# Performance work log

Measured on AMD Instinct MI355X. Metric: run time of the kernel, lower is better.

Reference implementation:

```python
import jax, jax.numpy as jnp
import numpy as np

B, S, D, H, T, R = 2, 2048, 768, 12, 64, 50
DH = D // H
EPS = 1e-12


def setup_inputs() -> dict:
    key = jax.random.key(0)
    ks = jax.random.split(key, 12)
    w = lambda k, shape: jax.random.normal(k, shape, jnp.float32) * 0.02
    inp = {
        "hidden_states": jax.random.normal(ks[0], (B, S, D), jnp.float32),
        "tag_emb": w(ks[1], (T, D)),
        "sa_wq": w(ks[2], (D, D)), "sa_bq": jnp.zeros((D,), jnp.float32),
        "sa_wk": w(ks[3], (D, D)), "sa_bk": jnp.zeros((D,), jnp.float32),
        "sa_wv": w(ks[4], (D, D)), "sa_bv": jnp.zeros((D,), jnp.float32),
        "sa_wo": w(ks[5], (D, D)), "sa_bo": jnp.zeros((D,), jnp.float32),
        "sa_ln_g": jnp.ones((D,), jnp.float32), "sa_ln_b": jnp.zeros((D,), jnp.float32),
        "ca_wq": w(ks[6], (D, D)), "ca_bq": jnp.zeros((D,), jnp.float32),
        "ca_wk": w(ks[7], (D, D)), "ca_bk": jnp.zeros((D,), jnp.float32),
        "ca_wv": w(ks[8], (D, D)), "ca_bv": jnp.zeros((D,), jnp.float32),
        "ca_wo": w(ks[9], (D, D)), "ca_bo": jnp.zeros((D,), jnp.float32),
        "ca_ln_g": jnp.ones((D,), jnp.float32), "ca_ln_b": jnp.zeros((D,), jnp.float32),
        "ff_w1": w(ks[10], (D, 3072)), "ff_b1": jnp.zeros((3072,), jnp.float32),
        "ff_w2": w(ks[11], (3072, D)), "ff_b2": jnp.zeros((D,), jnp.float32),
        "ff_ln_g": jnp.ones((D,), jnp.float32), "ff_ln_b": jnp.zeros((D,), jnp.float32),
    }
    return inp


def _layernorm(x, g, b):
    m = jnp.mean(x, axis=-1, keepdims=True)
    v = jnp.mean(jnp.square(x - m), axis=-1, keepdims=True)
    return (x - m) * jax.lax.rsqrt(v + EPS) * g + b


def _bert_attention(x, kv, mask, wq, bq, wk, bk, wv, bv, wo, bo, ln_g, ln_b):
    # BertSelfAttention: multi-head attn; mask (if any) is ADDED to scores (HF semantics).
    Bq, Sq = x.shape[0], x.shape[1]
    Sk = kv.shape[1]
    q = (x @ wq + bq).reshape(Bq, Sq, H, DH)
    k = (kv @ wk + bk).reshape(Bq, Sk, H, DH)
    v = (kv @ wv + bv).reshape(Bq, Sk, H, DH)
    scores = jnp.einsum("bqhd,bkhd->bhqk", q, k) / jnp.sqrt(jnp.float32(DH))
    if mask is not None:
        scores = scores + mask  # additive 0/1 band mask, as in the source
    probs = jax.nn.softmax(scores, axis=-1)
    ctx = jnp.einsum("bhqk,bkhd->bqhd", probs, v).reshape(Bq, Sq, D)
    # BertSelfOutput: dense + residual + LayerNorm
    return _layernorm(ctx @ wo + bo + x, ln_g, ln_b)


def reference(hidden_states, tag_emb,
              sa_wq, sa_bq, sa_wk, sa_bk, sa_wv, sa_bv, sa_wo, sa_bo, sa_ln_g, sa_ln_b,
              ca_wq, ca_bq, ca_wk, ca_bk, ca_wv, ca_bv, ca_wo, ca_bo, ca_ln_g, ca_ln_b,
              ff_w1, ff_b1, ff_w2, ff_b2, ff_ln_g, ff_ln_b):
    Sd = hidden_states.shape[1]
    # banded mask: tril(+R) * triu(-R) -> 1 inside window, 0 outside (added to scores)
    i = jnp.arange(Sd)
    band = (jnp.abs(i[:, None] - i[None, :]) <= R).astype(hidden_states.dtype)  # [S,S]
    attn_out = _bert_attention(hidden_states, hidden_states, band,
                               sa_wq, sa_bq, sa_wk, sa_bk, sa_wv, sa_bv,
                               sa_wo, sa_bo, sa_ln_g, sa_ln_b)
    tags = jnp.broadcast_to(tag_emb[None], (hidden_states.shape[0], T, D))
    attn_out = _bert_attention(attn_out, tags, None,
                               ca_wq, ca_bq, ca_wk, ca_bk, ca_wv, ca_bv,
                               ca_wo, ca_bo, ca_ln_g, ca_ln_b)
    # BertIntermediate + BertOutput (exact erf gelu as in HF)
    inter = jax.nn.gelu(attn_out @ ff_w1 + ff_b1, approximate=False)
    return _layernorm(inter @ ff_w2 + ff_b2 + attn_out, ff_ln_g, ff_ln_b)
```

## Files before the change

### kernel.cpp

```cpp
#include <hip/hip_runtime.h>
#include <cstdint>
#include <cstddef>


typedef __bf16 bf16;
typedef __bf16 bf16x8 __attribute__((ext_vector_type(8)));
typedef __bf16 bf16x4 __attribute__((ext_vector_type(4)));
typedef __bf16 bf16x2 __attribute__((ext_vector_type(2)));
typedef float  floatx4 __attribute__((ext_vector_type(4)));

__device__ __forceinline__ void glds16(const bf16* g, bf16* l) {
  __builtin_amdgcn_global_load_lds((const __attribute__((address_space(1))) void*)g,
                                   (__attribute__((address_space(3))) void*)l, 16, 0, 0);
}

__device__ __forceinline__ float fexp2(float x) {
  float r;
  asm("v_exp_f32 %0, %1" : "=v"(r) : "v"(x));
  return r;
}

__global__ __launch_bounds__(256) void k_prep(const float* __restrict__ sa_bq,
                                              const float* __restrict__ sa_bk,
                                              const float* __restrict__ sa_bv,
                                              const float* __restrict__ ca_bk,
                                              const float* __restrict__ ca_bv,
                                              const float* __restrict__ tag,
                                              float* __restrict__ bQKV,
                                              float* __restrict__ bKV2,
                                              bf16* __restrict__ tagp) {
  int b = blockIdx.x, t = threadIdx.x;
  if (b < 9) {
    int i = b * 256 + t;
    int s = i / 768, j = i - s * 768;
    const float* p = s == 0 ? sa_bq : (s == 1 ? sa_bk : sa_bv);
    bQKV[i] = p[j];
  } else if (b < 15) {
    int i = (b - 9) * 256 + t;
    int s = i / 768, j = i - s * 768;
    bKV2[i] = s == 0 ? ca_bk[j] : ca_bv[j];
  } else {
    int i = (b - 15) * 256 + t;
    if (i < 64 * 768) tagp[i] = (bf16)tag[i];
    else tagp[i] = (bf16)0.f;
  }
}

__global__ __launch_bounds__(256) void k_precast(const float* __restrict__ X,
                                                 bf16* __restrict__ Xb) {
  int i = (blockIdx.x * 256 + threadIdx.x) * 8;
  float4 a = *(const float4*)(X + i);
  float4 b4 = *(const float4*)(X + i + 4);
  bf16x8 o;
  o[0] = (bf16)a.x; o[1] = (bf16)a.y; o[2] = (bf16)a.z; o[3] = (bf16)a.w;
  o[4] = (bf16)b4.x; o[5] = (bf16)b4.y; o[6] = (bf16)b4.z; o[7] = (bf16)b4.w;
  *(bf16x8*)(Xb + i) = o;
}

__global__ __launch_bounds__(256) void k_transpose(const float* __restrict__ W,
                                                   bf16* __restrict__ Wt,
                                                   int K, int N) {
  __shared__ bf16 tile[64][72];
  int n0 = blockIdx.x * 64, k0 = blockIdx.y * 64;
  int t = threadIdx.x;
  int r = t >> 2, cg = (t & 3) * 16;
  const float* src = W + (size_t)(k0 + r) * N + n0 + cg;
  float tmp[16];
  *(float4*)&tmp[0]  = *(const float4*)(src);
  *(float4*)&tmp[4]  = *(const float4*)(src + 4);
  *(float4*)&tmp[8]  = *(const float4*)(src + 8);
  *(float4*)&tmp[12] = *(const float4*)(src + 12);
#pragma unroll
  for (int i = 0; i < 16; ++i) tile[r][cg + i] = (bf16)tmp[i];
  __syncthreads();
  bf16* dst = Wt + (size_t)(n0 + r) * K + k0 + cg;
#pragma unroll
  for (int g = 0; g < 2; ++g) {
    bf16x8 pack;
#pragma unroll
    for (int i = 0; i < 8; ++i) pack[i] = tile[cg + g * 8 + i][r];
    *(bf16x8*)(dst + g * 8) = pack;
  }
}

__global__ __launch_bounds__(256) void k_transpose4(const float* __restrict__ W0,
                                                    const float* __restrict__ W1,
                                                    const float* __restrict__ W2w,
                                                    const float* __restrict__ W3,
                                                    bf16* __restrict__ Wt) {
  __shared__ bf16 tile[64][72];
  int z = blockIdx.z;
  const float* W = z == 0 ? W0 : (z == 1 ? W1 : (z == 2 ? W2w : W3));
  bf16* dstb = Wt + (size_t)z * 768 * 768;
  int n0 = blockIdx.x * 64, k0 = blockIdx.y * 64;
  int t = threadIdx.x;
  int r = t >> 2, cg = (t & 3) * 16;
  const float* src = W + (size_t)(k0 + r) * 768 + n0 + cg;
  float tmp[16];
  *(float4*)&tmp[0]  = *(const float4*)(src);
  *(float4*)&tmp[4]  = *(const float4*)(src + 4);
  *(float4*)&tmp[8]  = *(const float4*)(src + 8);
  *(float4*)&tmp[12] = *(const float4*)(src + 12);
#pragma unroll
  for (int i = 0; i < 16; ++i) tile[r][cg + i] = (bf16)tmp[i];
  __syncthreads();
  bf16* dst = dstb + (size_t)(n0 + r) * 768 + k0 + cg;
#pragma unroll
  for (int g = 0; g < 2; ++g) {
    bf16x8 pack;
#pragma unroll
    for (int i = 0; i < 8; ++i) pack[i] = tile[cg + g * 8 + i][r];
    *(bf16x8*)(dst + g * 8) = pack;
  }
}

template <int BM, int BN, int KS, bool CF32>
__global__ __launch_bounds__(256) void k_gemm(const bf16* __restrict__ Ab,
                                              const bf16* __restrict__ Bt,
                                              const float* __restrict__ bias,
                                              void* __restrict__ Cv,
                                              void* __restrict__ Cv2,
                                              int M, int N, int K, int ld, int act) {
  constexpr int MT = BM / 32;
  constexpr int NT = BN / 32;
  __shared__ bf16 As[KS][BM * 32];
  __shared__ bf16 Bs[KS][BN * 32];
  int tid = threadIdx.x;
  int lane = tid & 63, wave = tid >> 6;
  int l16 = lane & 15, quad = lane >> 4;
  int wm = wave & 1, wn = wave >> 1;
  int m0 = blockIdx.x * BM, n0 = blockIdx.y * BN;
  int z = blockIdx.z;
  int arow = tid >> 2, acol = (tid & 3) * 8;
  int ldst = arow * 32 + acol;

  const bf16* Ap = Ab + (size_t)(m0 + arow) * ld + z * K + acol;
  const bf16* Bp = Bt + (size_t)(n0 + arow) * ld + z * K + acol;

  floatx4 acc[MT][NT];
#pragma unroll
  for (int i = 0; i < MT; ++i)
#pragma unroll
    for (int j = 0; j < NT; ++j) acc[i][j] = floatx4{0.f, 0.f, 0.f, 0.f};

  for (int k = 0; k < K; k += 32 * KS) {
    __syncthreads();
#pragma unroll
    for (int ks = 0; ks < KS; ++ks) {
      glds16(Bp + k + ks * 32, &Bs[ks][ldst]);
      if constexpr (BN == 128) glds16(Bp + (size_t)64 * ld + k + ks * 32, &Bs[ks][ldst + 2048]);
      glds16(Ap + k + ks * 32, &As[ks][ldst]);
      if constexpr (BM == 128) glds16(Ap + (size_t)64 * ld + k + ks * 32, &As[ks][ldst + 2048]);
    }
    __syncthreads();
#pragma unroll
    for (int ks = 0; ks < KS; ++ks) {
      bf16x8 a_frag[MT], b_frag[NT];
#pragma unroll
      for (int mt = 0; mt < MT; ++mt)
        a_frag[mt] = *(const bf16x8*)&As[ks][(wm * (BM / 2) + mt * 16 + l16) * 32 + quad * 8];
#pragma unroll
      for (int nt = 0; nt < NT; ++nt)
        b_frag[nt] = *(const bf16x8*)&Bs[ks][(wn * (BN / 2) + nt * 16 + l16) * 32 + quad * 8];
#pragma unroll
      for (int mt = 0; mt < MT; ++mt)
#pragma unroll
        for (int nt = 0; nt < NT; ++nt)
          acc[mt][nt] = __builtin_amdgcn_mfma_f32_16x16x32_bf16(a_frag[mt], b_frag[nt], acc[mt][nt], 0, 0, 0);
    }
  }

  void* Co = (z == 0) ? Cv : Cv2;
#pragma unroll
  for (int nt = 0; nt < NT; ++nt) {
    int col = n0 + wn * (BN / 2) + nt * 16 + l16;
    float bv = (z == 0) ? bias[col] : 0.f;
#pragma unroll
    for (int mt = 0; mt < MT; ++mt) {
#pragma unroll
      for (int r = 0; r < 4; ++r) {
        int row = m0 + wm * (BM / 2) + mt * 16 + quad * 4 + r;
        float v = acc[mt][nt][r] + bv;
        if (act) v = 0.5f * v * (1.f + erff(v * 0.70710678118654752f));
        if constexpr (CF32) ((float*)Co)[(size_t)row * N + col] = v;
        else ((bf16*)Co)[(size_t)row * N + col] = (bf16)v;
      }
    }
  }
}

__global__ __launch_bounds__(256) void k_attn_mfma(const bf16* __restrict__ Q, int ldq,
                                                   const bf16* __restrict__ Kp,
                                                   const bf16* __restrict__ Vp, int ldkv,
                                                   bf16* __restrict__ O,
                                                   int S, int Skv,
                                                   long long kv_bstride, int bandR) {
  const int NH = 12;
  int qt = blockIdx.x, bh = blockIdx.y;
  int bb = bh / NH, h = bh % NH;
  const bf16* Qb = Q + (size_t)bb * S * ldq + h * 64;
  const bf16* Kb = Kp + (size_t)bb * kv_bstride + h * 64;
  const bf16* Vb = Vp + (size_t)bb * kv_bstride + h * 64;
  bf16* Ob = O + (size_t)bb * S * 768 + h * 64;

  __shared__ __align__(16) char smem[47104];
  float* Obuf = (float*)smem;
  float* l0_arr = (float*)(smem + 16896);

  int tid = threadIdx.x, wave = tid >> 6, lane = tid & 63;
  int quad = lane >> 4, l16 = lane & 15;
  int qh = wave & 1, kh = wave >> 1;
  bf16 (*Psw)[40] = (bf16(*)[40])(smem + 36864 + wave * 2560);

  const float C1 = 0.18033688f;
  const float C2 = 1.44269504f;

  int r = tid >> 2, cg = (tid & 3) * 16;
  int vk0 = 2 * (tid & 31);
  int vd0 = 8 * (tid >> 5);
  int vcol = (vk0 + 16 * (vd0 >> 4)) & 63;

  bf16x8 aq[2][2];
#pragma unroll
  for (int mt = 0; mt < 2; ++mt) {
    const bf16* qsrc = Qb + (size_t)(qt * 64 + qh * 32 + mt * 16 + l16) * ldq;
#pragma unroll
    for (int ks = 0; ks < 2; ++ks) {
      bf16x8 t = *(const bf16x8*)(qsrc + ks * 32 + quad * 8);
#pragma unroll
      for (int e = 0; e < 8; ++e) t[e] = (bf16)((float)t[e] * C1);
      aq[mt][ks] = t;
    }
  }

  bf16x8 kr0, kr1, vr0, vr1;
  {
    const bf16* ksrc = Kb + (size_t)r * ldkv + cg;
    kr0 = *(const bf16x8*)ksrc;
    kr1 = *(const bf16x8*)(ksrc + 8);
    const bf16* vsrc = Vb + (size_t)vk0 * ldkv + vd0;
    vr0 = *(const bf16x8*)vsrc;
    vr1 = *(const bf16x8*)(vsrc + ldkv);
  }

  float l_part[2][4];
  floatx4 acc[2][4];
#pragma unroll
  for (int mt = 0; mt < 2; ++mt)
#pragma unroll
    for (int j = 0; j < 4; ++j) {
      l_part[mt][j] = 0.f;
      acc[mt][j] = floatx4{0.f, 0.f, 0.f, 0.f};
    }

  int qi0 = qt * 64 + qh * 32 + quad * 4;

  for (int kc = 0; kc < Skv; kc += 64) {
    int cur = (kc >> 6) & 1;
    bf16 (*Ks)[72] = (bf16(*)[72])(smem + cur * 9216);
    bf16 (*Vt)[72] = (bf16(*)[72])(smem + 18432 + cur * 9216);
    *(bf16x8*)&Ks[r][cg] = kr0;
    *(bf16x8*)&Ks[r][cg + 8] = kr1;
#pragma unroll
    for (int e = 0; e < 8; ++e) {
      bf16x2 p; p[0] = vr0[e]; p[1] = vr1[e];
      *(bf16x2*)&Vt[vd0 + e][vcol] = p;
    }
    if (kc + 64 < Skv) {
      const bf16* ksrc = Kb + (size_t)(kc + 64 + r) * ldkv + cg;
      kr0 = *(const bf16x8*)ksrc;
      kr1 = *(const bf16x8*)(ksrc + 8);
      const bf16* vsrc = Vb + (size_t)(kc + 64 + vk0) * ldkv + vd0;
      vr0 = *(const bf16x8*)vsrc;
      vr1 = *(const bf16x8*)(vsrc + ldkv);
    }
    __syncthreads();

    floatx4 s[2][2];
    __builtin_amdgcn_s_setprio(1);
#pragma unroll
    for (int kt = 0; kt < 2; ++kt) {
      bf16x8 bk0 = *(const bf16x8*)&Ks[kh * 32 + kt * 16 + l16][quad * 8];
      bf16x8 bk1 = *(const bf16x8*)&Ks[kh * 32 + kt * 16 + l16][32 + quad * 8];
#pragma unroll
      for (int mt = 0; mt < 2; ++mt) {
        floatx4 c = {0.f, 0.f, 0.f, 0.f};
        c = __builtin_amdgcn_mfma_f32_16x16x32_bf16(aq[mt][0], bk0, c, 0, 0, 0);
        c = __builtin_amdgcn_mfma_f32_16x16x32_bf16(aq[mt][1], bk1, c, 0, 0, 0);
        s[mt][kt] = c;
      }
    }
    __builtin_amdgcn_s_setprio(0);

    bool masked = (bandR >= 0) && (kc <= qt * 64 + 63 + bandR) &&
                  (kc + 63 >= qt * 64 - bandR);
    if (masked) {
#pragma unroll
      for (int kt = 0; kt < 2; ++kt) {
        int kj = kc + kh * 32 + kt * 16 + l16;
        int colp = (kt * 16 + l16 + 8 * quad) & 31;
#pragma unroll
        for (int mt = 0; mt < 2; ++mt)
#pragma unroll
          for (int rr = 0; rr < 4; ++rr) {
            int d = qi0 + mt * 16 + rr - kj; if (d < 0) d = -d;
            float e = fexp2(s[mt][kt][rr] + (d <= bandR ? C2 : 0.f));
            l_part[mt][rr] += e;
            Psw[mt * 16 + quad * 4 + rr][colp] = (bf16)e;
          }
      }
    } else {
#pragma unroll
      for (int kt = 0; kt < 2; ++kt) {
        int colp = (kt * 16 + l16 + 8 * quad) & 31;
#pragma unroll
        for (int mt = 0; mt < 2; ++mt)
#pragma unroll
          for (int rr = 0; rr < 4; ++rr) {
            float e = fexp2(s[mt][kt][rr]);
            l_part[mt][rr] += e;
            Psw[mt * 16 + quad * 4 + rr][colp] = (bf16)e;
          }
      }
    }

    bf16x8 ap[2];
#pragma unroll
    for (int mt = 0; mt < 2; ++mt)
      ap[mt] = *(const bf16x8*)&Psw[mt * 16 + l16][8 * ((quad + (l16 >> 2)) & 3)];
    __builtin_amdgcn_s_setprio(1);
#pragma unroll
    for (int nt = 0; nt < 4; ++nt) {
      bf16x8 bv = *(const bf16x8*)&Vt[nt * 16 + l16][(kh * 32 + quad * 8 + 16 * nt) & 63];
#pragma unroll
      for (int mt = 0; mt < 2; ++mt)
        acc[mt][nt] = __builtin_amdgcn_mfma_f32_16x16x32_bf16(ap[mt], bv, acc[mt][nt], 0, 0, 0);
    }
    __builtin_amdgcn_s_setprio(0);
  }

  float lr[2][4];
#pragma unroll
  for (int mt = 0; mt < 2; ++mt)
#pragma unroll
    for (int rr = 0; rr < 4; ++rr) {
      float t = l_part[mt][rr];
      t += __shfl_xor(t, 1);
      t += __shfl_xor(t, 2);
      t += __shfl_xor(t, 4);
      t += __shfl_xor(t, 8);
      lr[mt][rr] = t;
    }
  __syncthreads();
  if (kh == 0) {
#pragma unroll
    for (int mt = 0; mt < 2; ++mt)
#pragma unroll
      for (int nt = 0; nt < 4; ++nt)
#pragma unroll
        for (int rr = 0; rr < 4; ++rr)
          Obuf[(qh * 32 + mt * 16 + quad * 4 + rr) * 66 + nt * 16 + l16] = acc[mt][nt][rr];
    if (l16 == 0) {
#pragma unroll
      for (int mt = 0; mt < 2; ++mt)
#pragma unroll
        for (int rr = 0; rr < 4; ++rr)
          l0_arr[qh * 32 + mt * 16 + quad * 4 + rr] = lr[mt][rr];
    }
  }
  __syncthreads();
  if (kh == 1) {
#pragma unroll
    for (int mt = 0; mt < 2; ++mt)
#pragma unroll
      for (int rr = 0; rr < 4; ++rr) {
        int ql = qh * 32 + mt * 16 + quad * 4 + rr;
        float lt = lr[mt][rr] + l0_arr[ql];
        int qrow = qt * 64 + ql;
#pragma unroll
        for (int nt = 0; nt < 4; ++nt) {
          float o = (acc[mt][nt][rr] + Obuf[ql * 66 + nt * 16 + l16]) / lt;
          Ob[(size_t)qrow * 768 + nt * 16 + l16] = (bf16)o;
        }
      }
  }
}

template <typename TY, typename TR, typename TO>
__global__ __launch_bounds__(256) void k_add_ln(const TY* __restrict__ Y,
                                                const TR* __restrict__ X,
                                                const float* __restrict__ Y2,
                                                const float* __restrict__ g,
                                                const float* __restrict__ b,
                                                TO* __restrict__ out) {
  int wave = threadIdx.x >> 6, lane = threadIdx.x & 63;
  int row = blockIdx.x * 4 + wave;
  const TY* y = Y + (size_t)row * 768;
  const TR* x = X + (size_t)row * 768;
  float v[12];
  float s = 0.f, s2 = 0.f;
#pragma unroll
  for (int c = 0; c < 3; ++c) {
    int idx = c * 256 + lane * 4;
    float yv[4], xv[4];
    if constexpr (__is_same(TY, float)) {
      float4 t = *(const float4*)(y + idx);
      yv[0] = t.x; yv[1] = t.y; yv[2] = t.z; yv[3] = t.w;
    } else {
      bf16x4 t = *(const bf16x4*)(y + idx);
#pragma unroll
      for (int i = 0; i < 4; ++i) yv[i] = (float)t[i];
    }
    if constexpr (__is_same(TR, float)) {
      float4 t = *(const float4*)(x + idx);
      xv[0] = t.x; xv[1] = t.y; xv[2] = t.z; xv[3] = t.w;
    } else {
      bf16x4 t = *(const bf16x4*)(x + idx);
#pragma unroll
      for (int i = 0; i < 4; ++i) xv[i] = (float)t[i];
    }
    if (Y2 != nullptr) {
      float4 t2 = *(const float4*)(Y2 + (size_t)row * 768 + idx);
      xv[0] += t2.x; xv[1] += t2.y; xv[2] += t2.z; xv[3] += t2.w;
    }
#pragma unroll
    for (int i = 0; i < 4; ++i) {
      float t = yv[i] + xv[i];
      v[c * 4 + i] = t; s += t; s2 += t * t;
    }
  }
#pragma unroll
  for (int off = 32; off > 0; off >>= 1) { s += __shfl_xor(s, off); s2 += __shfl_xor(s2, off); }
  float mean = s * (1.f / 768.f);
  float var = fmaxf(s2 * (1.f / 768.f) - mean * mean, 0.f);
  float inv = rsqrtf(var + 1e-12f);
  TO* o = out + (size_t)row * 768;
#pragma unroll
  for (int c = 0; c < 3; ++c) {
    int idx = c * 256 + lane * 4;
    float4 gv = *(const float4*)(g + idx);
    float4 bv = *(const float4*)(b + idx);
    float r0 = (v[c * 4 + 0] - mean) * inv * gv.x + bv.x;
    float r1 = (v[c * 4 + 1] - mean) * inv * gv.y + bv.y;
    float r2 = (v[c * 4 + 2] - mean) * inv * gv.z + bv.z;
    float r3 = (v[c * 4 + 3] - mean) * inv * gv.w + bv.w;
    if constexpr (__is_same(TO, float)) {
      float4 ov = {r0, r1, r2, r3};
      *(float4*)(o + idx) = ov;
    } else {
      bf16x4 ov;
      ov[0] = (bf16)r0; ov[1] = (bf16)r1; ov[2] = (bf16)r2; ov[3] = (bf16)r3;
      *(bf16x4*)(o + idx) = ov;
    }
  }
}

extern "C" void kernel_launch(void* const* d_in, const int* in_sizes, int n_in,
                              void* d_out, int out_size, void* d_ws, size_t ws_size,
                              hipStream_t stream) {
  (void)in_sizes; (void)n_in; (void)out_size; (void)ws_size;
  const float* X     = (const float*)d_in[0];
  const float* tag   = (const float*)d_in[1];
  const float* sa_wq = (const float*)d_in[2];
  const float* sa_bq = (const float*)d_in[3];
  const float* sa_wk = (const float*)d_in[4];
  const float* sa_bk = (const float*)d_in[5];
  const float* sa_wv = (const float*)d_in[6];
  const float* sa_bv = (const float*)d_in[7];
  const float* sa_wo = (const float*)d_in[8];
  const float* sa_bo = (const float*)d_in[9];
  const float* sa_lg = (const float*)d_in[10];
  const float* sa_lb = (const float*)d_in[11];
  const float* ca_wq = (const float*)d_in[12];
  const float* ca_bq = (const float*)d_in[13];
  const float* ca_wk = (const float*)d_in[14];
  const float* ca_bk = (const float*)d_in[15];
  const float* ca_wv = (const float*)d_in[16];
  const float* ca_bv = (const float*)d_in[17];
  const float* ca_wo = (const float*)d_in[18];
  const float* ca_bo = (const float*)d_in[19];
  const float* ca_lg = (const float*)d_in[20];
  const float* ca_lb = (const float*)d_in[21];
  const float* ff_w1 = (const float*)d_in[22];
  const float* ff_b1 = (const float*)d_in[23];
  const float* ff_w2 = (const float*)d_in[24];
  const float* ff_b2 = (const float*)d_in[25];
  const float* ff_lg = (const float*)d_in[26];
  const float* ff_lb = (const float*)d_in[27];

  float* outf = (float*)d_out;
  bf16* outb = (bf16*)d_out;
  const size_t SLOT = (size_t)4096 * 768;

  bf16* BIG   = (bf16*)d_ws;
  bf16* slotA = BIG + (size_t)4096 * 2304;
  bf16* Wall  = slotA + SLOT;
  bf16* W2    = Wall + (size_t)3072 * 768;
  bf16* tagp  = W2;
  bf16* k2v2  = W2 + (size_t)128 * 768;
  float* bQKV = (float*)(W2 + (size_t)128 * 768 + (size_t)128 * 1536);
  float* bKV2 = bQKV + 2304;
  float* P1   = (float*)(BIG + 2 * SLOT);
  bf16*  Xb   = outb + SLOT;

  dim3 blk(256);

  k_prep<<<dim3(399), blk, 0, stream>>>(sa_bq, sa_bk, sa_bv, ca_bk, ca_bv, tag,
                                        bQKV, bKV2, tagp);
  k_precast<<<dim3(1536), blk, 0, stream>>>(X, Xb);

  k_transpose4<<<dim3(12, 12, 4), blk, 0, stream>>>(sa_wq, sa_wk, sa_wv, sa_wo, Wall);
  k_gemm<64, 64, 4, false><<<dim3(64, 36), blk, 0, stream>>>(Xb, Wall, bQKV, BIG, nullptr,
                                                             4096, 2304, 768, 768, 0);
  k_attn_mfma<<<dim3(32, 24), blk, 0, stream>>>(BIG, 2304, BIG + 768, BIG + 1536, 2304,
                                                outb, 2048, 2048, (long long)2048 * 2304, 50);
  k_gemm<64, 64, 4, false><<<dim3(64, 12), blk, 0, stream>>>(outb, Wall + (size_t)2304 * 768,
                                                             sa_bo, slotA, nullptr,
                                                             4096, 768, 768, 768, 0);
  k_add_ln<bf16, float, bf16><<<dim3(1024), blk, 0, stream>>>(slotA, X, nullptr, sa_lg, sa_lb, slotA);

  k_transpose4<<<dim3(12, 12, 4), blk, 0, stream>>>(ca_wq, ca_wk, ca_wv, ca_wo, Wall);
  k_gemm<64, 64, 4, false><<<dim3(64, 12), blk, 0, stream>>>(slotA, Wall, ca_bq, BIG, nullptr,
                                                             4096, 768, 768, 768, 0);
  k_gemm<64, 64, 4, false><<<dim3(2, 24), blk, 0, stream>>>(tagp, Wall + (size_t)768 * 768,
                                                            bKV2, k2v2, nullptr,
                                                            128, 1536, 768, 768, 0);
  k_attn_mfma<<<dim3(32, 24), blk, 0, stream>>>(BIG, 768, k2v2, k2v2 + 768, 1536,
                                                outb, 2048, 64, 0, -1);
  k_gemm<64, 64, 4, false><<<dim3(64, 12), blk, 0, stream>>>(outb, Wall + (size_t)2304 * 768,
                                                             ca_bo, BIG + SLOT, nullptr,
                                                             4096, 768, 768, 768, 0);
  k_add_ln<bf16, bf16, bf16><<<dim3(1024), blk, 0, stream>>>(BIG + SLOT, slotA, nullptr,
                                                             ca_lg, ca_lb, slotA);

  k_transpose<<<dim3(48, 12), blk, 0, stream>>>(ff_w1, Wall, 768, 3072);
  k_transpose<<<dim3(12, 48), blk, 0, stream>>>(ff_w2, W2, 3072, 768);
  for (int mc = 0; mc < 2; ++mc) {
    const bf16* a2 = slotA + (size_t)mc * 2048 * 768;
    float* yo = outf + (size_t)mc * 2048 * 768;
    k_gemm<64, 128, 4, false><<<dim3(32, 24), blk, 0, stream>>>(a2, Wall, ff_b1, BIG, nullptr,
                                                                2048, 3072, 768, 768, 1);
    k_gemm<64, 64, 4, true><<<dim3(32, 12, 2), blk, 0, stream>>>(BIG, W2, ff_b2, yo, P1,
                                                                 2048, 768, 1536, 3072, 0);
    k_add_ln<float, bf16, float><<<dim3(512), blk, 0, stream>>>(yo, a2, P1, ff_lg, ff_lb, yo);
  }
}
```

Measured before the change: 397.4 us.

## Merge prep/precast, transposes and Q2/KV2 GEMMs; retile QKV and FF1 GEMMs

Merges the bias/tag prep and the input bf16 cast into one launch. It also merges the two FF weight transposes into one launch and the cross-attention Q and tag K/V projections into one grid, reducing kernel launches and tail gaps. The QKV and FF1 GEMMs switch to 128x64 tiles with two K-stages, and the cross-attention weight transpose moves ahead of the first LayerNorm. The retiling changes LDS use per block and grid occupancy, and the merged Q2KV grid launches many idle blocks that return early.

```diff
diff --git a/kernel.cpp b/kernel.cpp
--- a/kernel.cpp
+++ b/kernel.cpp
@@ -20,15 +20,17 @@
   return r;
 }
 
-__global__ __launch_bounds__(256) void k_prep(const float* __restrict__ sa_bq,
-                                              const float* __restrict__ sa_bk,
-                                              const float* __restrict__ sa_bv,
-                                              const float* __restrict__ ca_bk,
-                                              const float* __restrict__ ca_bv,
-                                              const float* __restrict__ tag,
-                                              float* __restrict__ bQKV,
-                                              float* __restrict__ bKV2,
-                                              bf16* __restrict__ tagp) {
+__global__ __launch_bounds__(256) void k_prep_all(const float* __restrict__ sa_bq,
+                                                  const float* __restrict__ sa_bk,
+                                                  const float* __restrict__ sa_bv,
+                                                  const float* __restrict__ ca_bk,
+                                                  const float* __restrict__ ca_bv,
+                                                  const float* __restrict__ tag,
+                                                  const float* __restrict__ X,
+                                                  float* __restrict__ bQKV,
+                                                  float* __restrict__ bKV2,
+                                                  bf16* __restrict__ tagp,
+                                                  bf16* __restrict__ Xb) {
   int b = blockIdx.x, t = threadIdx.x;
   if (b < 9) {
     int i = b * 256 + t;
@@ -39,29 +41,25 @@
     int i = (b - 9) * 256 + t;
     int s = i / 768, j = i - s * 768;
     bKV2[i] = s == 0 ? ca_bk[j] : ca_bv[j];
-  } else {
+  } else if (b < 399) {
     int i = (b - 15) * 256 + t;
     if (i < 64 * 768) tagp[i] = (bf16)tag[i];
     else tagp[i] = (bf16)0.f;
-  }
-}
-
-__global__ __launch_bounds__(256) void k_precast(const float* __restrict__ X,
-                                                 bf16* __restrict__ Xb) {
-  int i = (blockIdx.x * 256 + threadIdx.x) * 8;
-  float4 a = *(const float4*)(X + i);
-  float4 b4 = *(const float4*)(X + i + 4);
-  bf16x8 o;
-  o[0] = (bf16)a.x; o[1] = (bf16)a.y; o[2] = (bf16)a.z; o[3] = (bf16)a.w;
-  o[4] = (bf16)b4.x; o[5] = (bf16)b4.y; o[6] = (bf16)b4.z; o[7] = (bf16)b4.w;
-  *(bf16x8*)(Xb + i) = o;
-}
-
-__global__ __launch_bounds__(256) void k_transpose(const float* __restrict__ W,
-                                                   bf16* __restrict__ Wt,
-                                                   int K, int N) {
-  __shared__ bf16 tile[64][72];
-  int n0 = blockIdx.x * 64, k0 = blockIdx.y * 64;
+  } else {
+    int i = ((b - 399) * 256 + t) * 8;
+    float4 a = *(const float4*)(X + i);
+    float4 b4 = *(const float4*)(X + i + 4);
+    bf16x8 o;
+    o[0] = (bf16)a.x; o[1] = (bf16)a.y; o[2] = (bf16)a.z; o[3] = (bf16)a.w;
+    o[4] = (bf16)b4.x; o[5] = (bf16)b4.y; o[6] = (bf16)b4.z; o[7] = (bf16)b4.w;
+    *(bf16x8*)(Xb + i) = o;
+  }
+}
+
+__device__ __forceinline__ void transpose_body(const float* __restrict__ W,
+                                               bf16* __restrict__ Wt,
+                                               int K, int N, int n0, int k0,
+                                               bf16 (*tile)[72]) {
   int t = threadIdx.x;
   int r = t >> 2, cg = (t & 3) * 16;
   const float* src = W + (size_t)(k0 + r) * N + n0 + cg;
@@ -91,51 +89,41 @@
   __shared__ bf16 tile[64][72];
   int z = blockIdx.z;
   const float* W = z == 0 ? W0 : (z == 1 ? W1 : (z == 2 ? W2w : W3));
-  bf16* dstb = Wt + (size_t)z * 768 * 768;
-  int n0 = blockIdx.x * 64, k0 = blockIdx.y * 64;
-  int t = threadIdx.x;
-  int r = t >> 2, cg = (t & 3) * 16;
-  const float* src = W + (size_t)(k0 + r) * 768 + n0 + cg;
-  float tmp[16];
-  *(float4*)&tmp[0]  = *(const float4*)(src);
-  *(float4*)&tmp[4]  = *(const float4*)(src + 4);
-  *(float4*)&tmp[8]  = *(const float4*)(src + 8);
-  *(float4*)&tmp[12] = *(const float4*)(src + 12);
-#pragma unroll
-  for (int i = 0; i < 16; ++i) tile[r][cg + i] = (bf16)tmp[i];
-  __syncthreads();
-  bf16* dst = dstb + (size_t)(n0 + r) * 768 + k0 + cg;
-#pragma unroll
-  for (int g = 0; g < 2; ++g) {
-    bf16x8 pack;
-#pragma unroll
-    for (int i = 0; i < 8; ++i) pack[i] = tile[cg + g * 8 + i][r];
-    *(bf16x8*)(dst + g * 8) = pack;
-  }
+  transpose_body(W, Wt + (size_t)z * 768 * 768, 768, 768,
+                 blockIdx.x * 64, blockIdx.y * 64, tile);
+}
+
+__global__ __launch_bounds__(256) void k_transpose_ff(const float* __restrict__ ff_w1,
+                                                      const float* __restrict__ ff_w2,
+                                                      bf16* __restrict__ Wall,
+                                                      bf16* __restrict__ W2) {
+  __shared__ bf16 tile[64][72];
+  if (blockIdx.z == 0)
+    transpose_body(ff_w1, Wall, 768, 3072, blockIdx.x * 64, blockIdx.y * 64, tile);
+  else
+    transpose_body(ff_w2, W2, 3072, 768, blockIdx.y * 64, blockIdx.x * 64, tile);
 }
 
 template <int BM, int BN, int KS, bool CF32>
-__global__ __launch_bounds__(256) void k_gemm(const bf16* __restrict__ Ab,
-                                              const bf16* __restrict__ Bt,
-                                              const float* __restrict__ bias,
-                                              void* __restrict__ Cv,
-                                              void* __restrict__ Cv2,
-                                              int M, int N, int K, int ld, int act) {
+__device__ __forceinline__ void gemm_body(const bf16* __restrict__ Ab,
+                                          const bf16* __restrict__ Bt,
+                                          const float* __restrict__ bias,
+                                          void* __restrict__ Co,
+                                          int N, int K, int ld, int act,
+                                          int m0, int n0,
+                                          bf16* __restrict__ As,
+                                          bf16* __restrict__ Bs) {
   constexpr int MT = BM / 32;
   constexpr int NT = BN / 32;
-  __shared__ bf16 As[KS][BM * 32];
-  __shared__ bf16 Bs[KS][BN * 32];
   int tid = threadIdx.x;
   int lane = tid & 63, wave = tid >> 6;
   int l16 = lane & 15, quad = lane >> 4;
   int wm = wave & 1, wn = wave >> 1;
-  int m0 = blockIdx.x * BM, n0 = blockIdx.y * BN;
-  int z = blockIdx.z;
   int arow = tid >> 2, acol = (tid & 3) * 8;
   int ldst = arow * 32 + acol;
 
-  const bf16* Ap = Ab + (size_t)(m0 + arow) * ld + z * K + acol;
-  const bf16* Bp = Bt + (size_t)(n0 + arow) * ld + z * K + acol;
+  const bf16* Ap = Ab + (size_t)(m0 + arow) * ld + acol;
+  const bf16* Bp = Bt + (size_t)(n0 + arow) * ld + acol;
 
   floatx4 acc[MT][NT];
 #pragma unroll
@@ -147,10 +135,10 @@
     __syncthreads();
 #pragma unroll
     for (int ks = 0; ks < KS; ++ks) {
-      glds16(Bp + k + ks * 32, &Bs[ks][ldst]);
-      if constexpr (BN == 128) glds16(Bp + (size_t)64 * ld + k + ks * 32, &Bs[ks][ldst + 2048]);
-      glds16(Ap + k + ks * 32, &As[ks][ldst]);
-      if constexpr (BM == 128) glds16(Ap + (size_t)64 * ld + k + ks * 32, &As[ks][ldst + 2048]);
+      glds16(Bp + k + ks * 32, Bs + ks * BN * 32 + ldst);
+      if constexpr (BN == 128) glds16(Bp + (size_t)64 * ld + k + ks * 32, Bs + ks * BN * 32 + ldst + 2048);
+      glds16(Ap + k + ks * 32, As + ks * BM * 32 + ldst);
+      if constexpr (BM == 128) glds16(Ap + (size_t)64 * ld + k + ks * 32, As + ks * BM * 32 + ldst + 2048);
     }
     __syncthreads();
 #pragma unroll
@@ -158,10 +146,10 @@
       bf16x8 a_frag[MT], b_frag[NT];
 #pragma unroll
       for (int mt = 0; mt < MT; ++mt)
-        a_frag[mt] = *(const bf16x8*)&As[ks][(wm * (BM / 2) + mt * 16 + l16) * 32 + quad * 8];
+        a_frag[mt] = *(const bf16x8*)(As + ks * BM * 32 + (wm * (BM / 2) + mt * 16 + l16) * 32 + quad * 8);
 #pragma unroll
       for (int nt = 0; nt < NT; ++nt)
-        b_frag[nt] = *(const bf16x8*)&Bs[ks][(wn * (BN / 2) + nt * 16 + l16) * 32 + quad * 8];
+        b_frag[nt] = *(const bf16x8*)(Bs + ks * BN * 32 + (wn * (BN / 2) + nt * 16 + l16) * 32 + quad * 8);
 #pragma unroll
       for (int mt = 0; mt < MT; ++mt)
 #pragma unroll
@@ -170,11 +158,10 @@
     }
   }
 
-  void* Co = (z == 0) ? Cv : Cv2;
 #pragma unroll
   for (int nt = 0; nt < NT; ++nt) {
     int col = n0 + wn * (BN / 2) + nt * 16 + l16;
-    float bv = (z == 0) ? bias[col] : 0.f;
+    float bv = bias ? bias[col] : 0.f;
 #pragma unroll
     for (int mt = 0; mt < MT; ++mt) {
 #pragma unroll
@@ -186,6 +173,41 @@
         else ((bf16*)Co)[(size_t)row * N + col] = (bf16)v;
       }
     }
+  }
+}
+
+template <int BM, int BN, int KS, bool CF32>
+__global__ __launch_bounds__(256) void k_gemm(const bf16* __restrict__ Ab,
+                                              const bf16* __restrict__ Bt,
+                                              const float* __restrict__ bias,
+                                              void* __restrict__ Cv,
+                                              void* __restrict__ Cv2,
+                                              int N, int K, int ld, int act) {
+  __shared__ bf16 As[KS * BM * 32];
+  __shared__ bf16 Bs[KS * BN * 32];
+  int z = blockIdx.z;
+  gemm_body<BM, BN, KS, CF32>(Ab + z * K, Bt + z * K, z == 0 ? bias : nullptr,
+                              z == 0 ? Cv : Cv2, N, K, ld, act,
+                              blockIdx.x * BM, blockIdx.y * BN, As, Bs);
+}
+
+__global__ __launch_bounds__(256) void k_gemm_q2kv(const bf16* __restrict__ A0,
+                                                   const bf16* __restrict__ B0,
+                                                   const float* __restrict__ bias0,
+                                                   bf16* __restrict__ C0,
+                                                   const bf16* __restrict__ A1,
+                                                   const bf16* __restrict__ B1,
+                                                   const float* __restrict__ bias1,
+                                                   bf16* __restrict__ C1) {
+  __shared__ bf16 As[4 * 64 * 32];
+  __shared__ bf16 Bs[4 * 64 * 32];
+  if (blockIdx.z == 0) {
+    gemm_body<64, 64, 4, false>(A0, B0, bias0, C0, 768, 768, 768, 0,
+                                blockIdx.x * 64, blockIdx.y * 64, As, Bs);
+  } else {
+    if (blockIdx.y != 0 || blockIdx.x >= 48) return;
+    gemm_body<64, 64, 4, false>(A1, B1, bias1, C1, 1536, 768, 768, 0,
+                                (blockIdx.x & 1) * 64, (blockIdx.x >> 1) * 64, As, Bs);
   }
 }
 
@@ -505,43 +527,38 @@
 
   dim3 blk(256);
 
-  k_prep<<<dim3(399), blk, 0, stream>>>(sa_bq, sa_bk, sa_bv, ca_bk, ca_bv, tag,
-                                        bQKV, bKV2, tagp);
-  k_precast<<<dim3(1536), blk, 0, stream>>>(X, Xb);
+  k_prep_all<<<dim3(1935), blk, 0, stream>>>(sa_bq, sa_bk, sa_bv, ca_bk, ca_bv, tag, X,
+                                             bQKV, bKV2, tagp, Xb);
 
   k_transpose4<<<dim3(12, 12, 4), blk, 0, stream>>>(sa_wq, sa_wk, sa_wv, sa_wo, Wall);
-  k_gemm<64, 64, 4, false><<<dim3(64, 36), blk, 0, stream>>>(Xb, Wall, bQKV, BIG, nullptr,
-                                                             4096, 2304, 768, 768, 0);
+  k_gemm<128, 64, 2, false><<<dim3(32, 36), blk, 0, stream>>>(Xb, Wall, bQKV, BIG, nullptr,
+                                                              2304, 768, 768, 0);
   k_attn_mfma<<<dim3(32, 24), blk, 0, stream>>>(BIG, 2304, BIG + 768, BIG + 1536, 2304,
                                                 outb, 2048, 2048, (long long)2048 * 2304, 50);
   k_gemm<64, 64, 4, false><<<dim3(64, 12), blk, 0, stream>>>(outb, Wall + (size_t)2304 * 768,
                                                              sa_bo, slotA, nullptr,
-                                                             4096, 768, 768, 768, 0);
+                                                             768, 768, 768, 0);
+  k_transpose4<<<dim3(12, 12, 4), blk, 0, stream>>>(ca_wq, ca_wk, ca_wv, ca_wo, Wall);
   k_add_ln<bf16, float, bf16><<<dim3(1024), blk, 0, stream>>>(slotA, X, nullptr, sa_lg, sa_lb, slotA);
 
-  k_transpose4<<<dim3(12, 12, 4), blk, 0, stream>>>(ca_wq, ca_wk, ca_wv, ca_wo, Wall);
-  k_gemm<64, 64, 4, false><<<dim3(64, 12), blk, 0, stream>>>(slotA, Wall, ca_bq, BIG, nullptr,
-                                                             4096, 768, 768, 768, 0);
-  k_gemm<64, 64, 4, false><<<dim3(2, 24), blk, 0, stream>>>(tagp, Wall + (size_t)768 * 768,
-                                                            bKV2, k2v2, nullptr,
-                                                            128, 1536, 768, 768, 0);
+  k_gemm_q2kv<<<dim3(64, 12, 2), blk, 0, stream>>>(slotA, Wall, ca_bq, BIG,
+                                                   tagp, Wall + (size_t)768 * 768, bKV2, k2v2);
   k_attn_mfma<<<dim3(32, 24), blk, 0, stream>>>(BIG, 768, k2v2, k2v2 + 768, 1536,
                                                 outb, 2048, 64, 0, -1);
   k_gemm<64, 64, 4, false><<<dim3(64, 12), blk, 0, stream>>>(outb, Wall + (size_t)2304 * 768,
                                                              ca_bo, BIG + SLOT, nullptr,
-                                                             4096, 768, 768, 768, 0);
+                                                             768, 768, 768, 0);
   k_add_ln<bf16, bf16, bf16><<<dim3(1024), blk, 0, stream>>>(BIG + SLOT, slotA, nullptr,
                                                              ca_lg, ca_lb, slotA);
 
-  k_transpose<<<dim3(48, 12), blk, 0, stream>>>(ff_w1, Wall, 768, 3072);
-  k_transpose<<<dim3(12, 48), blk, 0, stream>>>(ff_w2, W2, 3072, 768);
+  k_transpose_ff<<<dim3(48, 12, 2), blk, 0, stream>>>(ff_w1, ff_w2, Wall, W2);
   for (int mc = 0; mc < 2; ++mc) {
     const bf16* a2 = slotA + (size_t)mc * 2048 * 768;
     float* yo = outf + (size_t)mc * 2048 * 768;
-    k_gemm<64, 128, 4, false><<<dim3(32, 24), blk, 0, stream>>>(a2, Wall, ff_b1, BIG, nullptr,
-                                                                2048, 3072, 768, 768, 1);
+    k_gemm<128, 64, 2, false><<<dim3(16, 48), blk, 0, stream>>>(a2, Wall, ff_b1, BIG, nullptr,
+                                                                3072, 768, 768, 1);
     k_gemm<64, 64, 4, true><<<dim3(32, 12, 2), blk, 0, stream>>>(BIG, W2, ff_b2, yo, P1,
-                                                                 2048, 768, 1536, 3072, 0);
+                                                                 768, 1536, 3072, 0);
     k_add_ln<float, bf16, float><<<dim3(512), blk, 0, stream>>>(yo, a2, P1, ff_lg, ff_lb, yo);
   }
 }
```

Result: faster. 387.4 us (-2.5%).
